# Performance work log

Measured on AMD Instinct MI355X. Metric: run time of the kernel, lower is better.

The kernel has to match this reference:

```python
import jax, jax.numpy as jnp
import numpy as np

B, D = 8192, 256      # batch, input_dim == n_nodes
ENC = 256             # encoder_dim
DEC = 64              # decoder_dim
THR = 0.1             # adjacency threshold


def setup_inputs() -> dict:
    key = jax.random.key(0)
    ks = jax.random.split(key, 9)
    s = lambda k, sh, fan: jax.random.normal(k, sh, jnp.float32) / np.sqrt(fan).astype(np.float32)
    return {
        "x": jax.random.normal(ks[0], (B, D), jnp.float32),
        "eps": jax.random.normal(ks[1], (B, D), jnp.float32),
        "W_enc": s(ks[2], (D, ENC), D), "b_enc": jnp.zeros((ENC,), jnp.float32),
        "W_mu": s(ks[3], (ENC, D), ENC), "b_mu": jnp.zeros((D,), jnp.float32),
        "W_lv": s(ks[4], (ENC, D), ENC), "b_lv": jnp.zeros((D,), jnp.float32),
        "graph_param": jax.random.normal(ks[5], (D, D), jnp.float32),
        "W_emb": s(ks[6], (D, DEC), 1), "b_emb": jnp.zeros((D, DEC), jnp.float32),
        "W_g1": s(ks[7], (DEC, DEC // 2), DEC), "b_g1": jnp.zeros((DEC // 2,), jnp.float32),
        "W_g2": s(ks[8], (DEC // 2, 1), DEC // 2), "b_g2": jnp.zeros((1,), jnp.float32),
        "iter_": 100,
    }


def _learned_graph(graph_param, iter_):
    # LearnedGraph.forward: sigmoid, force self-loops=1, threshold after iter 50
    g = jax.nn.sigmoid(graph_param)
    eye = jnp.eye(g.shape[0], dtype=g.dtype)
    g = g * (1.0 - eye) + eye
    if iter_ > 50:  # iter_ is a static Python int
        g = jnp.where(g > THR, g, 0.0)  # nn.Threshold(THR, 0)
    return g


def _gcn_norm(adj):
    # DGL GraphConv(norm='both') with edge_weight: messages weighted by adj values,
    # but degree normalization uses structural (unweighted) edge counts.
    mask = (adj != 0).astype(adj.dtype)
    dout = jnp.maximum(mask.sum(1), 1.0)  # out-degree of src j (row sums)
    din = jnp.maximum(mask.sum(0), 1.0)   # in-degree of dst i (col sums)
    # out[i] = sum_j adj[j,i] * x[j] / sqrt(dout[j] * din[i])  ->  M[dst, src]
    return (adj / jnp.sqrt(dout)[:, None] / jnp.sqrt(din)[None, :]).T


def reference(x, eps, W_enc, b_enc, W_mu, b_mu, W_lv, b_lv,
              graph_param, W_emb, b_emb, W_g1, b_g1, W_g2, b_g2, iter_):
    # VAE encoder (Linear + ReLU, then mu/logvar heads)
    h = jax.nn.relu(x @ W_enc + b_enc)
    mu = h @ W_mu + b_mu
    logvar = h @ W_lv + b_lv
    z = mu + eps * jnp.exp(0.5 * logvar)                 # [B, D]
    # learned adjacency over the D feature-nodes
    adj = _learned_graph(graph_param, iter_)             # [D, D]
    # per-feature node embedding: Linear(1, DEC) + tanh per feature
    b_z = jnp.tanh(z[:, :, None] * W_emb[None] + b_emb[None])  # [B, D, DEC]
    # two GraphConv layers (shared adjacency per batch element)
    M = _gcn_norm(adj)                                   # [D, D]
    h1 = jax.nn.relu(jnp.einsum('ij,bjd->bid', M, b_z) @ W_g1 + b_g1)  # [B, D, 32]
    h2 = jnp.einsum('ij,bjd->bid', M, h1) @ W_g2 + b_g2                # [B, D, 1]
    x_hat = h2.reshape(B, -1)                            # [B, D]
    return x_hat, adj, mu, logvar
```

## Files before the change

kernel.cpp:

```cpp
#include <hip/hip_runtime.h>

typedef __bf16 bf16_t;
typedef __bf16 bf16x4 __attribute__((ext_vector_type(4)));
typedef __bf16 bf16x8 __attribute__((ext_vector_type(8)));
typedef float  floatx4 __attribute__((ext_vector_type(4)));
typedef unsigned long long u64;

#define MFMA16(a, b, c) __builtin_amdgcn_mfma_f32_16x16x32_bf16((a), (b), (c), 0, 0, 0)

#define ADJ_OFF  2097152
#define MU_OFF   2162688
#define LV_OFF   4259840

#define TWO_LOG2E 2.8853900817779268f

__device__ __forceinline__ float fast_tanh2(float argE2) {
    float e = __builtin_amdgcn_exp2f(argE2);
    return 1.0f - 2.0f * __builtin_amdgcn_rcpf(e + 1.0f);
}

__device__ __forceinline__ bf16x8 cvt8(const float* p) {
    const floatx4 a = *(const floatx4*)p;
    const floatx4 b = *(const floatx4*)(p + 4);
    bf16x8 r;
#pragma unroll
    for (int j = 0; j < 4; j++) { r[j] = (bf16_t)a[j]; r[4 + j] = (bf16_t)b[j]; }
    return r;
}

__global__ __launch_bounds__(256) void k_prep(
    const float* __restrict__ We, const float* __restrict__ Wm,
    const float* __restrict__ Wl, const float* __restrict__ Wemb,
    const float* __restrict__ bemb, const float* __restrict__ gp,
    const int* __restrict__ iterp, bf16_t* __restrict__ Wt,
    bf16_t* __restrict__ wepack, bf16_t* __restrict__ bepack,
    u64* __restrict__ rowbits) {
    __shared__ float tile[32][33];
    const int b = blockIdx.x, tid = threadIdx.x;
    if (b < 192) {
        const int m = b >> 6, t6 = b & 63;
        const int K0 = (t6 >> 3) << 5, N0 = (t6 & 7) << 5;
        const float* src = (m == 0) ? We : ((m == 1) ? Wm : Wl);
#pragma unroll
        for (int p = 0; p < 4; p++) {
            const int idx = p * 256 + tid;
            tile[idx >> 5][idx & 31] = src[(K0 + (idx >> 5)) * 256 + N0 + (idx & 31)];
        }
        __syncthreads();
        bf16_t* dst = Wt + m * 65536;
#pragma unroll
        for (int p = 0; p < 4; p++) {
            const int idx = p * 256 + tid;
            const int nn = idx >> 5, kk = idx & 31;
            dst[(N0 + nn) * 256 + K0 + kk] = (bf16_t)tile[kk][nn];
        }
    } else if (b < 200) {
        const int base = (b - 192) * 2048;
#pragma unroll
        for (int p = 0; p < 8; p++) {
            const int idx = base + p * 256 + tid;
            wepack[idx] = (bf16_t)(TWO_LOG2E * Wemb[idx]);
        }
    } else if (b < 208) {
        const int base = (b - 200) * 2048;
#pragma unroll
        for (int p = 0; p < 8; p++) {
            const int idx = base + p * 256 + tid;
            bepack[idx] = (bf16_t)(TWO_LOG2E * bemb[idx]);
        }
    } else {
        const int j = b - 208;
        const bool thr = (*iterp) > 50;
        float g = 1.0f / (1.0f + expf(-gp[j * 256 + tid]));
        if (tid == j) g = 1.0f;
        if (thr && !(g > 0.1f)) g = 0.0f;
        const u64 bal = __ballot(g != 0.0f);
        if ((tid & 63) == 0) rowbits[j * 4 + (tid >> 6)] = bal;
    }
}

__global__ __launch_bounds__(256) void k_mkM(
    const float* __restrict__ gp, const int* __restrict__ iterp,
    const u64* __restrict__ rowbits, bf16_t* __restrict__ Mb,
    float* __restrict__ adjOut) {
    __shared__ u64 bits[256][4];
    const int j = blockIdx.x, t = threadIdx.x;
#pragma unroll
    for (int p = 0; p < 4; p++) {
        const int idx = p * 256 + t;
        bits[idx >> 2][idx & 3] = rowbits[idx];
    }
    __syncthreads();
    const int w64 = t >> 6, sh = t & 63;
    int cnt = 0;
#pragma unroll 8
    for (int jp = 0; jp < 256; jp++)
        cnt += (int)((bits[jp][w64] >> sh) & 1ull);
    const int rc = (int)(__popcll(bits[j][0]) + __popcll(bits[j][1]) +
                         __popcll(bits[j][2]) + __popcll(bits[j][3]));
    const float rso = rsqrtf((float)(rc < 1 ? 1 : rc));
    const float rsi = rsqrtf((float)(cnt < 1 ? 1 : cnt));
    float g = 1.0f / (1.0f + expf(-gp[j * 256 + t]));
    if (t == j) g = 1.0f;
    if ((*iterp) > 50 && !(g > 0.1f)) g = 0.0f;
    if (adjOut) adjOut[j * 256 + t] = g;
    Mb[t * 256 + j] = (bf16_t)(g * rso * rsi);
}

__global__ __launch_bounds__(512) void k_ench(
    const float* __restrict__ X, const bf16_t* __restrict__ Wt,
    const float* __restrict__ benc, const float* __restrict__ bmu,
    const float* __restrict__ blv,
    float* __restrict__ MuOut, float* __restrict__ LvOut) {
    __shared__ __align__(16) bf16_t Xs[32 * 264];
    __shared__ __align__(16) bf16_t Hs[32 * 264];
    const bf16_t* Bte = Wt;
    const bf16_t* Btm = Wt + 65536;
    const bf16_t* Btl = Wt + 131072;
    const int tid = threadIdx.x;
    const int r0 = blockIdx.x * 32;
    const int w = tid >> 6;
    const int lane = tid & 63;
    const int n = lane & 15, q = lane >> 4;
    const int cw = w * 32;
    const floatx4 z4 = {0.f, 0.f, 0.f, 0.f};

#pragma unroll
    for (int p = 0; p < 2; p++) {
        const int e0 = (p * 512 + tid) * 8;
        const int row = e0 >> 8, col = e0 & 255;
        *(bf16x8*)(Xs + row * 264 + col) = cvt8(X + (r0 + row) * 256 + col);
    }
    __syncthreads();

    floatx4 ah[2][2];
#pragma unroll
    for (int rt = 0; rt < 2; rt++)
#pragma unroll
        for (int tc = 0; tc < 2; tc++) ah[rt][tc] = z4;
#pragma unroll 2
    for (int k0 = 0; k0 < 256; k0 += 32) {
        bf16x8 a[2], b[2];
#pragma unroll
        for (int rt = 0; rt < 2; rt++)
            a[rt] = *(const bf16x8*)(Xs + (rt * 16 + n) * 264 + k0 + q * 8);
#pragma unroll
        for (int tc = 0; tc < 2; tc++)
            b[tc] = *(const bf16x8*)(Bte + (cw + tc * 16 + n) * 256 + k0 + q * 8);
#pragma unroll
        for (int rt = 0; rt < 2; rt++)
#pragma unroll
            for (int tc = 0; tc < 2; tc++)
                ah[rt][tc] = MFMA16(a[rt], b[tc], ah[rt][tc]);
    }
#pragma unroll
    for (int tc = 0; tc < 2; tc++) {
        const int col = cw + tc * 16 + n;
        const float bv = benc[col];
#pragma unroll
        for (int rt = 0; rt < 2; rt++)
#pragma unroll
            for (int r = 0; r < 4; r++)
                Hs[(rt * 16 + q * 4 + r) * 264 + col] =
                    (bf16_t)fmaxf(ah[rt][tc][r] + bv, 0.0f);
    }
    __syncthreads();

    floatx4 am[2][2], al[2][2];
#pragma unroll
    for (int rt = 0; rt < 2; rt++)
#pragma unroll
        for (int tc = 0; tc < 2; tc++) { am[rt][tc] = z4; al[rt][tc] = z4; }
#pragma unroll 2
    for (int k0 = 0; k0 < 256; k0 += 32) {
        bf16x8 a[2], bm_[2], bl_[2];
#pragma unroll
        for (int rt = 0; rt < 2; rt++)
            a[rt] = *(const bf16x8*)(Hs + (rt * 16 + n) * 264 + k0 + q * 8);
#pragma unroll
        for (int tc = 0; tc < 2; tc++) {
            bm_[tc] = *(const bf16x8*)(Btm + (cw + tc * 16 + n) * 256 + k0 + q * 8);
            bl_[tc] = *(const bf16x8*)(Btl + (cw + tc * 16 + n) * 256 + k0 + q * 8);
        }
#pragma unroll
        for (int rt = 0; rt < 2; rt++)
#pragma unroll
            for (int tc = 0; tc < 2; tc++) {
                am[rt][tc] = MFMA16(a[rt], bm_[tc], am[rt][tc]);
                al[rt][tc] = MFMA16(a[rt], bl_[tc], al[rt][tc]);
            }
    }
#pragma unroll
    for (int tc = 0; tc < 2; tc++) {
        const int col = cw + tc * 16 + n;
        const float bmv = bmu[col], blvv = blv[col];
#pragma unroll
        for (int rt = 0; rt < 2; rt++)
#pragma unroll
            for (int r = 0; r < 4; r++) {
                const int row = r0 + rt * 16 + q * 4 + r;
                MuOut[row * 256 + col] = am[rt][tc][r] + bmv;
                LvOut[row * 256 + col] = al[rt][tc][r] + blvv;
            }
    }
}

__global__ __launch_bounds__(512, 4) void k_gcn(
    const float* __restrict__ Mu, const float* __restrict__ Lv,
    const float* __restrict__ Eps, const bf16_t* __restrict__ wepack,
    const bf16_t* __restrict__ bepack, const float* __restrict__ Wg1,
    const float* __restrict__ bg1, const float* __restrict__ Wg2,
    const bf16_t* __restrict__ Mb, const float* __restrict__ bg2,
    float* __restrict__ xhat) {
    __shared__ __align__(16) bf16_t smem[128 * 256];
    __shared__ __align__(16) bf16_t Vs[4 * 256];
    __shared__ float zs[1024];
    const int tid = threadIdx.x;
    const int lane = tid & 63;
    const int w = tid >> 6;
    const int n = lane & 15, q = lane >> 4;
    const int bg = blockIdx.x;
    const floatx4 z4 = {0.f, 0.f, 0.f, 0.f};

    {
        const int gi = bg * 1024 + tid;
        zs[tid] = fmaf(Eps[gi], __expf(0.5f * Lv[gi]), Mu[gi]);
        const int gi2 = gi + 512;
        zs[tid + 512] = fmaf(Eps[gi2], __expf(0.5f * Lv[gi2]), Mu[gi2]);
    }

    bf16x8 wg1f[2][2];
#pragma unroll
    for (int ks = 0; ks < 2; ks++)
#pragma unroll
        for (int te = 0; te < 2; te++)
#pragma unroll
            for (int j = 0; j < 8; j++)
                wg1f[ks][te][j] = (bf16_t)Wg1[(ks * 32 + q * 8 + j) * 32 + te * 16 + n];
    __syncthreads();

#pragma unroll
    for (int jt2 = 0; jt2 < 2; jt2++) {
        const int j0 = (w * 2 + jt2) * 16;
        const int jA = j0 + n;
        const bf16x8 we0 = *(const bf16x8*)(wepack + jA * 64 + q * 8);
        const bf16x8 we1 = *(const bf16x8*)(wepack + jA * 64 + 32 + q * 8);
        const bf16x8 be0 = *(const bf16x8*)(bepack + jA * 64 + q * 8);
        const bf16x8 be1 = *(const bf16x8*)(bepack + jA * 64 + 32 + q * 8);
        const int j8a = (j0 >> 3) + (q >> 1);
        const int jlo = (q & 1) * 4;
        const int sw = ((j8a ^ (n & 7)) << 3) + jlo;
#pragma unroll
        for (int bl = 0; bl < 4; bl++) {
            const float zv = zs[bl * 256 + jA];
            bf16x8 a0, a1;
#pragma unroll
            for (int j = 0; j < 8; j++) {
                a0[j] = (bf16_t)fast_tanh2(fmaf(zv, (float)we0[j], (float)be0[j]));
                a1[j] = (bf16_t)fast_tanh2(fmaf(zv, (float)we1[j], (float)be1[j]));
            }
            floatx4 c0 = z4, c1 = z4;
            c0 = MFMA16(a0, wg1f[0][0], c0);
            c0 = MFMA16(a1, wg1f[1][0], c0);
            c1 = MFMA16(a0, wg1f[0][1], c1);
            c1 = MFMA16(a1, wg1f[1][1], c1);
            bf16x4 s0, s1;
#pragma unroll
            for (int r = 0; r < 4; r++) { s0[r] = (bf16_t)c0[r]; s1[r] = (bf16_t)c1[r]; }
            *(bf16x4*)(smem + (bl * 32 + n) * 256 + sw) = s0;
            *(bf16x4*)(smem + (bl * 32 + 16 + n) * 256 + sw) = s1;
        }
    }
    __syncthreads();

    const int i0 = w * 32;
    floatx4 acc[2][8];
#pragma unroll
    for (int ti = 0; ti < 2; ti++)
#pragma unroll
        for (int tc = 0; tc < 8; tc++) acc[ti][tc] = z4;
#pragma unroll
    for (int k0 = 0; k0 < 256; k0 += 32) {
        const int k8 = k0 >> 3;
        bf16x8 a[2], b[8];
#pragma unroll
        for (int ti = 0; ti < 2; ti++)
            a[ti] = *(const bf16x8*)(Mb + (i0 + ti * 16 + n) * 256 + k0 + q * 8);
#pragma unroll
        for (int tc = 0; tc < 8; tc++)
            b[tc] = *(const bf16x8*)(smem + (tc * 16 + n) * 256 +
                                     (((k8 + q) ^ (n & 7)) << 3));
        __builtin_amdgcn_s_setprio(1);
#pragma unroll
        for (int ti = 0; ti < 2; ti++)
#pragma unroll
            for (int tc = 0; tc < 8; tc++)
                acc[ti][tc] = MFMA16(a[ti], b[tc], acc[ti][tc]);
        __builtin_amdgcn_s_setprio(0);
    }

    const float w2a = Wg2[n],      w2b = Wg2[16 + n];
    const float b1a = bg1[n],      b1b = bg1[16 + n];
    float v32[32];
#pragma unroll
    for (int bl = 0; bl < 4; bl++)
#pragma unroll
        for (int ti = 0; ti < 2; ti++)
#pragma unroll
            for (int r = 0; r < 4; r++)
                v32[bl * 8 + ti * 4 + r] =
                    fmaxf(acc[ti][2 * bl][r] + b1a, 0.0f) * w2a +
                    fmaxf(acc[ti][2 * bl + 1][r] + b1b, 0.0f) * w2b;
    const bool h0 = (lane & 1), h1_ = (lane & 2), h2 = (lane & 4), h3 = (lane & 8);
    float u16[16];
#pragma unroll
    for (int p = 0; p < 16; p++) {
        const float keep = h0 ? v32[2 * p + 1] : v32[2 * p];
        const float send = h0 ? v32[2 * p] : v32[2 * p + 1];
        u16[p] = keep + __shfl_xor(send, 1, 64);
    }
    float u8[8];
#pragma unroll
    for (int p = 0; p < 8; p++) {
        const float keep = h1_ ? u16[2 * p + 1] : u16[2 * p];
        const float send = h1_ ? u16[2 * p] : u16[2 * p + 1];
        u8[p] = keep + __shfl_xor(send, 2, 64);
    }
    float u4[4];
#pragma unroll
    for (int p = 0; p < 4; p++) {
        const float keep = h2 ? u8[2 * p + 1] : u8[2 * p];
        const float send = h2 ? u8[2 * p] : u8[2 * p + 1];
        u4[p] = keep + __shfl_xor(send, 4, 64);
    }
    float u2[2];
#pragma unroll
    for (int p = 0; p < 2; p++) {
        const float keep = h3 ? u4[2 * p + 1] : u4[2 * p];
        const float send = h3 ? u4[2 * p] : u4[2 * p + 1];
        u2[p] = keep + __shfl_xor(send, 8, 64);
    }
    {
        const int i_out = i0 + ((n >> 2) & 1) * 16 + q * 4 + (n & 3);
        const int blv = n >> 3;
        Vs[blv * 256 + i_out] = (bf16_t)u2[0];
        Vs[(2 + blv) * 256 + i_out] = (bf16_t)u2[1];
    }
    __syncthreads();

    {
        floatx4 acc3[2];
        acc3[0] = z4; acc3[1] = z4;
#pragma unroll
        for (int k0 = 0; k0 < 256; k0 += 32) {
            const bf16x8 a3 = *(const bf16x8*)(Vs + (n & 3) * 256 + k0 + q * 8);
            bf16x8 b3[2];
#pragma unroll
            for (int tc = 0; tc < 2; tc++)
                b3[tc] = *(const bf16x8*)(Mb + (i0 + tc * 16 + n) * 256 + k0 + q * 8);
#pragma unroll
            for (int tc = 0; tc < 2; tc++)
                acc3[tc] = MFMA16(a3, b3[tc], acc3[tc]);
        }
        const float bv = bg2[0];
        if (q == 0) {
#pragma unroll
            for (int tc = 0; tc < 2; tc++)
#pragma unroll
                for (int r = 0; r < 4; r++)
                    xhat[(bg * 4 + r) * 256 + i0 + tc * 16 + n] = acc3[tc][r] + bv;
        }
    }
}

__global__ __launch_bounds__(256) void k_adj(
    const float* __restrict__ gp, const int* __restrict__ iterp,
    float* __restrict__ adjOut) {
    const int o = blockIdx.x * 256 + threadIdx.x;
    const int j = o >> 8, i = o & 255;
    float g = 1.0f / (1.0f + expf(-gp[o]));
    if (i == j) g = 1.0f;
    if ((*iterp) > 50 && !(g > 0.1f)) g = 0.0f;
    adjOut[o] = g;
}

extern "C" void kernel_launch(void* const* d_in, const int* in_sizes, int n_in,
                              void* d_out, int out_size, void* d_ws, size_t ws_size,
                              hipStream_t stream) {
    const float* x    = (const float*)d_in[0];
    const float* eps  = (const float*)d_in[1];
    const float* Wenc = (const float*)d_in[2];
    const float* benc = (const float*)d_in[3];
    const float* Wmu  = (const float*)d_in[4];
    const float* bmu  = (const float*)d_in[5];
    const float* Wlv  = (const float*)d_in[6];
    const float* blv  = (const float*)d_in[7];
    const float* gp   = (const float*)d_in[8];
    const float* Wemb = (const float*)d_in[9];
    const float* bemb = (const float*)d_in[10];
    const float* Wg1  = (const float*)d_in[11];
    const float* bg1  = (const float*)d_in[12];
    const float* Wg2  = (const float*)d_in[13];
    const float* bg2  = (const float*)d_in[14];
    const int*   itr  = (const int*)d_in[15];
    (void)in_sizes; (void)n_in; (void)out_size;

    float* xhat = (float*)d_out;
    float* adjO = xhat + ADJ_OFF;
    float* muo  = xhat + MU_OFF;
    float* lvo  = xhat + LV_OFF;

    const bool usews = (d_ws != nullptr && ws_size >= 262144);
    char* scr = usews ? (char*)d_ws : (char*)adjO;
    bf16_t* Mb      = (bf16_t*)scr;
    bf16_t* wepack  = (bf16_t*)(scr + 131072);
    bf16_t* bepack  = (bf16_t*)(scr + 163840);
    u64*    rowbits = (u64*)(scr + 196608);
    bf16_t* Wt      = (bf16_t*)((char*)d_out + 4194304);

    k_prep<<<dim3(464), dim3(256), 0, stream>>>(Wenc, Wmu, Wlv, Wemb, bemb,
                                                gp, itr, Wt, wepack, bepack,
                                                rowbits);
    k_mkM <<<dim3(256), dim3(256), 0, stream>>>(gp, itr, rowbits, Mb,
                                                usews ? adjO : nullptr);
    k_ench<<<dim3(256), dim3(512), 0, stream>>>(x, Wt, benc, bmu, blv, muo, lvo);
    k_gcn <<<dim3(2048), dim3(512), 0, stream>>>(muo, lvo, eps, wepack, bepack,
                                                 Wg1, bg1, Wg2, Mb, bg2, xhat);
    if (!usews)
        k_adj<<<dim3(256), dim3(256), 0, stream>>>(gp, itr, adjO);
}
```

Before: 207.0 us.

## Split final GCN matmul into separate batched kernel and enlarge encoder tiles

The final M·v product, which ran inside each GCN block on only 4 batch rows (a mostly wasted MFMA tile), moves to a new k_out kernel that processes 64 rows per block, reusing the xhat buffer for the intermediate vectors. The encoder kernel now handles 64 rows per block instead of 32 and computes the mu and logvar heads one after the other to hold register pressure down. The bf16-to-float weight conversions in the tanh loop are also hoisted out of the inner loop. The cost is an extra kernel launch plus an fp32 global round trip for the intermediate vector, and the encoder grid halves to 128 blocks, which may underfill the GPU.

```diff
diff --git a/kernel.cpp b/kernel.cpp
--- a/kernel.cpp
+++ b/kernel.cpp
@@ -112,13 +112,13 @@
     const float* __restrict__ benc, const float* __restrict__ bmu,
     const float* __restrict__ blv,
     float* __restrict__ MuOut, float* __restrict__ LvOut) {
-    __shared__ __align__(16) bf16_t Xs[32 * 264];
-    __shared__ __align__(16) bf16_t Hs[32 * 264];
+    __shared__ __align__(16) bf16_t Xs[64 * 264];
+    __shared__ __align__(16) bf16_t Hs[64 * 264];
     const bf16_t* Bte = Wt;
     const bf16_t* Btm = Wt + 65536;
     const bf16_t* Btl = Wt + 131072;
     const int tid = threadIdx.x;
-    const int r0 = blockIdx.x * 32;
+    const int r0 = blockIdx.x * 64;
     const int w = tid >> 6;
     const int lane = tid & 63;
     const int n = lane & 15, q = lane >> 4;
@@ -126,29 +126,29 @@
     const floatx4 z4 = {0.f, 0.f, 0.f, 0.f};
 
 #pragma unroll
-    for (int p = 0; p < 2; p++) {
+    for (int p = 0; p < 4; p++) {
         const int e0 = (p * 512 + tid) * 8;
         const int row = e0 >> 8, col = e0 & 255;
         *(bf16x8*)(Xs + row * 264 + col) = cvt8(X + (r0 + row) * 256 + col);
     }
     __syncthreads();
 
-    floatx4 ah[2][2];
-#pragma unroll
-    for (int rt = 0; rt < 2; rt++)
+    floatx4 ah[4][2];
+#pragma unroll
+    for (int rt = 0; rt < 4; rt++)
 #pragma unroll
         for (int tc = 0; tc < 2; tc++) ah[rt][tc] = z4;
 #pragma unroll 2
     for (int k0 = 0; k0 < 256; k0 += 32) {
-        bf16x8 a[2], b[2];
-#pragma unroll
-        for (int rt = 0; rt < 2; rt++)
+        bf16x8 a[4], b[2];
+#pragma unroll
+        for (int rt = 0; rt < 4; rt++)
             a[rt] = *(const bf16x8*)(Xs + (rt * 16 + n) * 264 + k0 + q * 8);
 #pragma unroll
         for (int tc = 0; tc < 2; tc++)
             b[tc] = *(const bf16x8*)(Bte + (cw + tc * 16 + n) * 256 + k0 + q * 8);
 #pragma unroll
-        for (int rt = 0; rt < 2; rt++)
+        for (int rt = 0; rt < 4; rt++)
 #pragma unroll
             for (int tc = 0; tc < 2; tc++)
                 ah[rt][tc] = MFMA16(a[rt], b[tc], ah[rt][tc]);
@@ -158,7 +158,7 @@
         const int col = cw + tc * 16 + n;
         const float bv = benc[col];
 #pragma unroll
-        for (int rt = 0; rt < 2; rt++)
+        for (int rt = 0; rt < 4; rt++)
 #pragma unroll
             for (int r = 0; r < 4; r++)
                 Hs[(rt * 16 + q * 4 + r) * 264 + col] =
@@ -166,42 +166,70 @@
     }
     __syncthreads();
 
-    floatx4 am[2][2], al[2][2];
-#pragma unroll
-    for (int rt = 0; rt < 2; rt++)
-#pragma unroll
-        for (int tc = 0; tc < 2; tc++) { am[rt][tc] = z4; al[rt][tc] = z4; }
+    {
+        floatx4 am[4][2];
+#pragma unroll
+        for (int rt = 0; rt < 4; rt++)
+#pragma unroll
+            for (int tc = 0; tc < 2; tc++) am[rt][tc] = z4;
 #pragma unroll 2
-    for (int k0 = 0; k0 < 256; k0 += 32) {
-        bf16x8 a[2], bm_[2], bl_[2];
-#pragma unroll
-        for (int rt = 0; rt < 2; rt++)
-            a[rt] = *(const bf16x8*)(Hs + (rt * 16 + n) * 264 + k0 + q * 8);
+        for (int k0 = 0; k0 < 256; k0 += 32) {
+            bf16x8 a[4], bm_[2];
+#pragma unroll
+            for (int rt = 0; rt < 4; rt++)
+                a[rt] = *(const bf16x8*)(Hs + (rt * 16 + n) * 264 + k0 + q * 8);
+#pragma unroll
+            for (int tc = 0; tc < 2; tc++)
+                bm_[tc] = *(const bf16x8*)(Btm + (cw + tc * 16 + n) * 256 + k0 + q * 8);
+#pragma unroll
+            for (int rt = 0; rt < 4; rt++)
+#pragma unroll
+                for (int tc = 0; tc < 2; tc++)
+                    am[rt][tc] = MFMA16(a[rt], bm_[tc], am[rt][tc]);
+        }
 #pragma unroll
         for (int tc = 0; tc < 2; tc++) {
-            bm_[tc] = *(const bf16x8*)(Btm + (cw + tc * 16 + n) * 256 + k0 + q * 8);
-            bl_[tc] = *(const bf16x8*)(Btl + (cw + tc * 16 + n) * 256 + k0 + q * 8);
-        }
-#pragma unroll
-        for (int rt = 0; rt < 2; rt++)
-#pragma unroll
-            for (int tc = 0; tc < 2; tc++) {
-                am[rt][tc] = MFMA16(a[rt], bm_[tc], am[rt][tc]);
-                al[rt][tc] = MFMA16(a[rt], bl_[tc], al[rt][tc]);
-            }
-    }
-#pragma unroll
-    for (int tc = 0; tc < 2; tc++) {
-        const int col = cw + tc * 16 + n;
-        const float bmv = bmu[col], blvv = blv[col];
-#pragma unroll
-        for (int rt = 0; rt < 2; rt++)
-#pragma unroll
-            for (int r = 0; r < 4; r++) {
-                const int row = r0 + rt * 16 + q * 4 + r;
-                MuOut[row * 256 + col] = am[rt][tc][r] + bmv;
-                LvOut[row * 256 + col] = al[rt][tc][r] + blvv;
-            }
+            const int col = cw + tc * 16 + n;
+            const float bmv = bmu[col];
+#pragma unroll
+            for (int rt = 0; rt < 4; rt++)
+#pragma unroll
+                for (int r = 0; r < 4; r++)
+                    MuOut[(r0 + rt * 16 + q * 4 + r) * 256 + col] = am[rt][tc][r] + bmv;
+        }
+    }
+
+    {
+        floatx4 al[4][2];
+#pragma unroll
+        for (int rt = 0; rt < 4; rt++)
+#pragma unroll
+            for (int tc = 0; tc < 2; tc++) al[rt][tc] = z4;
+#pragma unroll 2
+        for (int k0 = 0; k0 < 256; k0 += 32) {
+            bf16x8 a[4], bl_[2];
+#pragma unroll
+            for (int rt = 0; rt < 4; rt++)
+                a[rt] = *(const bf16x8*)(Hs + (rt * 16 + n) * 264 + k0 + q * 8);
+#pragma unroll
+            for (int tc = 0; tc < 2; tc++)
+                bl_[tc] = *(const bf16x8*)(Btl + (cw + tc * 16 + n) * 256 + k0 + q * 8);
+#pragma unroll
+            for (int rt = 0; rt < 4; rt++)
+#pragma unroll
+                for (int tc = 0; tc < 2; tc++)
+                    al[rt][tc] = MFMA16(a[rt], bl_[tc], al[rt][tc]);
+        }
+#pragma unroll
+        for (int tc = 0; tc < 2; tc++) {
+            const int col = cw + tc * 16 + n;
+            const float blvv = blv[col];
+#pragma unroll
+            for (int rt = 0; rt < 4; rt++)
+#pragma unroll
+                for (int r = 0; r < 4; r++)
+                    LvOut[(r0 + rt * 16 + q * 4 + r) * 256 + col] = al[rt][tc][r] + blvv;
+        }
     }
 }
 
@@ -210,10 +238,8 @@
     const float* __restrict__ Eps, const bf16_t* __restrict__ wepack,
     const bf16_t* __restrict__ bepack, const float* __restrict__ Wg1,
     const float* __restrict__ bg1, const float* __restrict__ Wg2,
-    const bf16_t* __restrict__ Mb, const float* __restrict__ bg2,
-    float* __restrict__ xhat) {
+    const bf16_t* __restrict__ Mb, float* __restrict__ Vout) {
     __shared__ __align__(16) bf16_t smem[128 * 256];
-    __shared__ __align__(16) bf16_t Vs[4 * 256];
     __shared__ float zs[1024];
     const int tid = threadIdx.x;
     const int lane = tid & 63;
@@ -247,6 +273,12 @@
         const bf16x8 we1 = *(const bf16x8*)(wepack + jA * 64 + 32 + q * 8);
         const bf16x8 be0 = *(const bf16x8*)(bepack + jA * 64 + q * 8);
         const bf16x8 be1 = *(const bf16x8*)(bepack + jA * 64 + 32 + q * 8);
+        float wf0[8], wf1[8], bf0[8], bf1[8];
+#pragma unroll
+        for (int j = 0; j < 8; j++) {
+            wf0[j] = (float)we0[j]; wf1[j] = (float)we1[j];
+            bf0[j] = (float)be0[j]; bf1[j] = (float)be1[j];
+        }
         const int j8a = (j0 >> 3) + (q >> 1);
         const int jlo = (q & 1) * 4;
         const int sw = ((j8a ^ (n & 7)) << 3) + jlo;
@@ -256,8 +288,8 @@
             bf16x8 a0, a1;
 #pragma unroll
             for (int j = 0; j < 8; j++) {
-                a0[j] = (bf16_t)fast_tanh2(fmaf(zv, (float)we0[j], (float)be0[j]));
-                a1[j] = (bf16_t)fast_tanh2(fmaf(zv, (float)we1[j], (float)be1[j]));
+                a0[j] = (bf16_t)fast_tanh2(fmaf(zv, wf0[j], bf0[j]));
+                a1[j] = (bf16_t)fast_tanh2(fmaf(zv, wf1[j], bf1[j]));
             }
             floatx4 c0 = z4, c1 = z4;
             c0 = MFMA16(a0, wg1f[0][0], c0);
@@ -343,33 +375,64 @@
     {
         const int i_out = i0 + ((n >> 2) & 1) * 16 + q * 4 + (n & 3);
         const int blv = n >> 3;
-        Vs[blv * 256 + i_out] = (bf16_t)u2[0];
-        Vs[(2 + blv) * 256 + i_out] = (bf16_t)u2[1];
-    }
-    __syncthreads();
-
-    {
-        floatx4 acc3[2];
-        acc3[0] = z4; acc3[1] = z4;
-#pragma unroll
-        for (int k0 = 0; k0 < 256; k0 += 32) {
-            const bf16x8 a3 = *(const bf16x8*)(Vs + (n & 3) * 256 + k0 + q * 8);
-            bf16x8 b3[2];
+        Vout[bg * 1024 + blv * 256 + i_out] = u2[0];
+        Vout[bg * 1024 + (2 + blv) * 256 + i_out] = u2[1];
+    }
+}
+
+__global__ __launch_bounds__(512) void k_out(
+    float* __restrict__ VX, const bf16_t* __restrict__ Mb,
+    const float* __restrict__ bg2) {
+    __shared__ __align__(16) bf16_t va[64 * 264];
+    const int tid = threadIdx.x;
+    const int lane = tid & 63;
+    const int w = tid >> 6;
+    const int n = lane & 15, q = lane >> 4;
+    const int r0 = blockIdx.x * 64;
+
+#pragma unroll
+    for (int p = 0; p < 8; p++) {
+        const int i4 = p * 512 + tid;
+        const int row = i4 >> 6, c4 = (i4 & 63) * 4;
+        const floatx4 v = *(const floatx4*)(VX + (r0 + row) * 256 + c4);
+        bf16x4 s;
+#pragma unroll
+        for (int r = 0; r < 4; r++) s[r] = (bf16_t)v[r];
+        *(bf16x4*)(va + row * 264 + c4) = s;
+    }
+    __syncthreads();
+
+    const int cw = w * 32;
+    const floatx4 z4 = {0.f, 0.f, 0.f, 0.f};
+    floatx4 acc[4][2];
+#pragma unroll
+    for (int rt = 0; rt < 4; rt++)
+#pragma unroll
+        for (int tc = 0; tc < 2; tc++) acc[rt][tc] = z4;
+#pragma unroll 2
+    for (int k0 = 0; k0 < 256; k0 += 32) {
+        bf16x8 a[4], b[2];
+#pragma unroll
+        for (int rt = 0; rt < 4; rt++)
+            a[rt] = *(const bf16x8*)(va + (rt * 16 + n) * 264 + k0 + q * 8);
+#pragma unroll
+        for (int tc = 0; tc < 2; tc++)
+            b[tc] = *(const bf16x8*)(Mb + (cw + tc * 16 + n) * 256 + k0 + q * 8);
+#pragma unroll
+        for (int rt = 0; rt < 4; rt++)
 #pragma unroll
             for (int tc = 0; tc < 2; tc++)
-                b3[tc] = *(const bf16x8*)(Mb + (i0 + tc * 16 + n) * 256 + k0 + q * 8);
-#pragma unroll
-            for (int tc = 0; tc < 2; tc++)
-                acc3[tc] = MFMA16(a3, b3[tc], acc3[tc]);
-        }
-        const float bv = bg2[0];
-        if (q == 0) {
-#pragma unroll
-            for (int tc = 0; tc < 2; tc++)
-#pragma unroll
-                for (int r = 0; r < 4; r++)
-                    xhat[(bg * 4 + r) * 256 + i0 + tc * 16 + n] = acc3[tc][r] + bv;
-        }
+                acc[rt][tc] = MFMA16(a[rt], b[tc], acc[rt][tc]);
+    }
+    const float bv = bg2[0];
+#pragma unroll
+    for (int tc = 0; tc < 2; tc++) {
+        const int col = cw + tc * 16 + n;
+#pragma unroll
+        for (int rt = 0; rt < 4; rt++)
+#pragma unroll
+            for (int r = 0; r < 4; r++)
+                VX[(r0 + rt * 16 + q * 4 + r) * 256 + col] = acc[rt][tc][r] + bv;
     }
 }
 
@@ -423,9 +486,10 @@
                                                 rowbits);
     k_mkM <<<dim3(256), dim3(256), 0, stream>>>(gp, itr, rowbits, Mb,
                                                 usews ? adjO : nullptr);
-    k_ench<<<dim3(256), dim3(512), 0, stream>>>(x, Wt, benc, bmu, blv, muo, lvo);
+    k_ench<<<dim3(128), dim3(512), 0, stream>>>(x, Wt, benc, bmu, blv, muo, lvo);
     k_gcn <<<dim3(2048), dim3(512), 0, stream>>>(muo, lvo, eps, wepack, bepack,
-                                                 Wg1, bg1, Wg2, Mb, bg2, xhat);
+                                                 Wg1, bg1, Wg2, Mb, xhat);
+    k_out <<<dim3(128), dim3(512), 0, stream>>>(xhat, Mb, bg2);
     if (!usews)
         k_adj<<<dim3(256), dim3(256), 0, stream>>>(gp, itr, adjO);
 }
```

After: 190.9 us. 7.8% less time.
